# Kernel tuning notes

Hardware: AMD Instinct MI355X
Metric: run time of the kernel (lower is better)

Reference implementation:

```python
import jax, jax.numpy as jnp
import numpy as np

N = 50000
E = 800000
H = 128

def setup_inputs() -> dict:
    key = jax.random.key(0)
    ks = jax.random.split(key, 12)
    s = 1.0 / np.sqrt(H)
    inp = {
        "x": jax.random.normal(ks[0], (N, H), dtype=jnp.float32),
        "edge_index": jax.random.randint(ks[1], (2, E), 0, N, dtype=jnp.int64),
        "edge_attr": jax.random.normal(ks[2], (E, H), dtype=jnp.float32),
        # linear_edge: Linear(3H, H)
        "We": jax.random.uniform(ks[3], (3 * H, H), jnp.float32, -s, s),
        "be": jnp.zeros((H,), jnp.float32),
        # attention_layer.W: Linear(H, H)
        "Wg": jax.random.uniform(ks[4], (H, H), jnp.float32, -s, s),
        "bg": jnp.zeros((H,), jnp.float32),
        # attention_layer.a: Linear(2H, 1)
        "Wa": jax.random.uniform(ks[5], (2 * H, 1), jnp.float32, -s, s),
        "ba": jnp.zeros((1,), jnp.float32),
        # linear_out: Linear(H, H)
        "Wo": jax.random.uniform(ks[6], (H, H), jnp.float32, -s, s),
        "bo": jnp.zeros((H,), jnp.float32),
    }
    return inp


def reference(x, edge_index, edge_attr, We, be, Wg, bg, Wa, ba, Wo, bo):
    # PyG MessagePassing (flow=source_to_target): j = edge_index[0] (source),
    # i = edge_index[1] (target); aggregation scatters to edge_index[1].
    src = edge_index[0]
    dst = edge_index[1]

    # message: SiLU(Linear(cat[x_i, x_j, edge_attr]))  -- split We to avoid a [E,3H] concat
    m = jax.nn.silu(x[dst] @ We[:H] + x[src] @ We[H:2 * H] + edge_attr @ We[2 * H:] + be)  # [E,H]
    agg = jax.ops.segment_sum(m, dst, num_segments=N)  # [N,H] scatter-add aggregate

    # GraphAttentionLayer: row, col = edge_index -> row=edge_index[0], col=edge_index[1]
    h = agg @ Wg + bg  # [N,H]
    score = jax.nn.leaky_relu(h[src] @ Wa[:H] + h[dst] @ Wa[H:] + ba, negative_slope=0.2)  # [E,1]
    # softmax over the last dim of size 1 -> all ones (faithful to original); dropout off (eval)
    alpha = jax.nn.softmax(score, axis=-1)  # [E,1]
    attn_out = jax.ops.segment_sum(alpha * h[dst], src, num_segments=N)  # [N,H]

    return attn_out @ Wo + bo  # linear_out
```

## Files before the change

### kernel.cpp

```cpp
#include <hip/hip_runtime.h>

#define N_NODES 50000
#define N_EDGES 800000

typedef unsigned short u16;
typedef unsigned int u32;
typedef __attribute__((ext_vector_type(8))) short short8;
typedef __attribute__((ext_vector_type(4))) float f32x4;
typedef __attribute__((ext_vector_type(2))) float f32x2;

__device__ __forceinline__ u16 f2bf(float f) {
    union { float f; u32 u; } v; v.f = f;
    u32 r = v.u + 0x7FFFu + ((v.u >> 16) & 1u);
    return (u16)(r >> 16);
}

__device__ __forceinline__ float bf2f(u16 h) {
    union { u32 u; float f; } v; v.u = ((u32)h) << 16;
    return v.f;
}

__global__ __launch_bounds__(256) void compute_wc(const float* __restrict__ Wg,
                                                  const float* __restrict__ bg,
                                                  const float* __restrict__ Wo,
                                                  float* __restrict__ Wc,
                                                  float* __restrict__ bc) {
    int b = blockIdx.x;
    if (b < 8) {
        for (int i = 0; i < 8; ++i) {
            int o = b * 2048 + i * 256 + threadIdx.x;
            int k = o >> 7, n = o & 127;
            float s = 0.f;
            for (int j = 0; j < 128; ++j) s += Wg[k * 128 + j] * Wo[j * 128 + n];
            Wc[o] = s;
        }
    } else if (threadIdx.x < 128) {
        int n = threadIdx.x;
        float s = 0.f;
        for (int j = 0; j < 128; ++j) s += bg[j] * Wo[j * 128 + n];
        bc[n] = s;
    }
}

__global__ __launch_bounds__(256) void pack_all(const float* __restrict__ We,
                                                const float* __restrict__ Wc,
                                                u16* __restrict__ PB1,
                                                u16* __restrict__ PBe,
                                                u16* __restrict__ PBc) {
    int bid = blockIdx.x;
    int job = bid >> 3;
    int t = bid & 7;
    const float* src; u16* dst; int slotBase, CH;
    if (job == 0)      { src = We;         dst = PB1; slotBase = 0; CH = 4; }
    else if (job == 1) { src = We + 32768; dst = PBe; slotBase = 0; CH = 8; }
    else if (job == 2) { src = We + 16384; dst = PBe; slotBase = 4; CH = 8; }
    else               { src = Wc;         dst = PBc; slotBase = 0; CH = 4; }
    int c = threadIdx.x >> 6;
    int lane = threadIdx.x & 63;
    int q = lane >> 4, n = lane & 15;
    const float* s = src + (size_t)(c * 32 + q * 8) * 128 + t * 16 + n;
    u16* dp = dst + (((size_t)(t * CH + slotBase + c) * 64 + lane) * 8);
#pragma unroll
    for (int j = 0; j < 8; ++j) dp[j] = f2bf(s[(size_t)j * 128]);
}

__global__ __launch_bounds__(256) void cast_bf16(const float* __restrict__ x,
                                                 u16* __restrict__ X2) {
    size_t i = (size_t)(blockIdx.x * 256 + threadIdx.x) * 8;
    f32x4 v0 = *(const f32x4*)(x + i);
    f32x4 v1 = *(const f32x4*)(x + i + 4);
    short8 o;
#pragma unroll
    for (int j = 0; j < 4; ++j) { o[j] = (short)f2bf(v0[j]); o[4 + j] = (short)f2bf(v1[j]); }
    *(short8*)(X2 + i) = o;
}

__global__ __launch_bounds__(256) void hist_kernel(const int* __restrict__ srcIdx,
                                                   const int* __restrict__ dstIdx,
                                                   int* __restrict__ degD,
                                                   int* __restrict__ degS) {
    int e = blockIdx.x * 256 + threadIdx.x;
    if (e >= N_EDGES) return;
    atomicAdd(&degD[dstIdx[e]], 1);
    atomicAdd(&degS[srcIdx[e]], 1);
}

__global__ __launch_bounds__(256) void scan_kernel(const int* __restrict__ degD,
                                                   const int* __restrict__ degS,
                                                   int* __restrict__ offD, int* __restrict__ curD,
                                                   int* __restrict__ offS, int* __restrict__ curS) {
    const int* deg = blockIdx.x ? degS : degD;
    int* off = blockIdx.x ? offS : offD;
    int* cur = blockIdx.x ? curS : curD;
    __shared__ int buf[256];
    const int CHUNK = 196;
    int tid = threadIdx.x;
    int s0 = tid * CHUNK, s1 = s0 + CHUNK;
    if (s1 > N_NODES) s1 = N_NODES;
    int s = 0;
    for (int i = s0; i < s1; ++i) s += deg[i];
    buf[tid] = s;
    __syncthreads();
    for (int o = 1; o < 256; o <<= 1) {
        int v = (tid >= o) ? buf[tid - o] : 0;
        __syncthreads();
        buf[tid] += v;
        __syncthreads();
    }
    int run = (tid > 0) ? buf[tid - 1] : 0;
    for (int i = s0; i < s1; ++i) {
        off[i] = run;
        cur[i] = run;
        run += deg[i];
    }
    if (tid == 255) off[N_NODES] = buf[255];
}

__global__ __launch_bounds__(256) void scatter_kernel(const int* __restrict__ srcIdx,
                                                      const int* __restrict__ dstIdx,
                                                      int* __restrict__ curD,
                                                      int* __restrict__ curS,
                                                      int2* __restrict__ sdP,
                                                      int* __restrict__ ss_dst) {
    int e = blockIdx.x * 256 + threadIdx.x;
    if (e >= N_EDGES) return;
    int s = srcIdx[e], d = dstIdx[e];
    int p = atomicAdd(&curD[d], 1);
    sdP[p] = make_int2(e, s);
    int p2 = atomicAdd(&curS[s], 1);
    ss_dst[p2] = d;
}

__global__ __launch_bounds__(256) void gemm_mfma(const void* __restrict__ Ap,
                                                 const u16* __restrict__ PB,
                                                 const float* __restrict__ bias,
                                                 const float* __restrict__ bias2,
                                                 const int* __restrict__ rowdeg,
                                                 void* __restrict__ outp,
                                                 int M, int Ctiles, int flags) {
    int tid = threadIdx.x;
    int wave = tid >> 6;
    int lane = tid & 63;
    int strip = blockIdx.x * 4 + wave;
    int row0 = strip * 16;
    if (row0 >= M) return;
    int q = lane >> 4, n = lane & 15;
    int C = Ctiles * 16;

    short8 a[4];
    if (flags & 2) {
        const u16* ap = (const u16*)Ap + (size_t)(row0 + n) * 128 + q * 8;
#pragma unroll
        for (int c = 0; c < 4; ++c) a[c] = *(const short8*)(ap + c * 32);
    } else {
        const float* ap = (const float*)Ap + (size_t)(row0 + n) * 128 + q * 8;
#pragma unroll
        for (int c = 0; c < 4; ++c) {
            f32x4 f0 = *(const f32x4*)(ap + c * 32);
            f32x4 f1 = *(const f32x4*)(ap + c * 32 + 4);
            short8 t;
#pragma unroll
            for (int j = 0; j < 4; ++j) {
                t[j] = (short)f2bf(f0[j]);
                t[4 + j] = (short)f2bf(f1[j]);
            }
            a[c] = t;
        }
    }

    float rb[4] = {0.f, 0.f, 0.f, 0.f};
    if (flags & 4) {
#pragma unroll
        for (int r = 0; r < 4; ++r) rb[r] = (float)rowdeg[row0 + q * 4 + r];
    }

    for (int t = 0; t < Ctiles; ++t) {
        f32x4 acc = {0.f, 0.f, 0.f, 0.f};
#pragma unroll
        for (int c = 0; c < 4; ++c) {
            short8 b = *(const short8*)(PB + (((size_t)t * 4 + c) * 64 + lane) * 8);
            acc = __builtin_amdgcn_mfma_f32_16x16x32_bf16(a[c], b, acc, 0, 0, 0);
        }
        int col = t * 16 + n;
        float bv = bias ? bias[col] : 0.f;
        float b2 = (flags & 4) ? bias2[col] : 0.f;
#pragma unroll
        for (int r = 0; r < 4; ++r) {
            int row = row0 + q * 4 + r;
            float v = acc[r] + bv + rb[r] * b2;
            if (flags & 1)
                ((u16*)outp)[(size_t)row * C + col] = f2bf(v);
            else
                ((float*)outp)[(size_t)row * C + col] = v;
        }
    }
}

__global__ __launch_bounds__(256) void agg_fused(const float* __restrict__ EA,
                                                 const u16* __restrict__ X2,
                                                 const u16* __restrict__ PBe,
                                                 const int* __restrict__ offD,
                                                 const int2* __restrict__ sdP,
                                                 const u16* __restrict__ T1a,
                                                 u16* __restrict__ agg) {
    int tid = threadIdx.x;
    int wave = tid >> 6;
    int lane = tid & 63;
    int node = blockIdx.x * 2 + (wave >> 1);
    if (node >= N_NODES) return;
    int cg = wave & 1;
    int q = lane >> 4, n = lane & 15;
    int segS = offD[node], segE = offD[node + 1];
    const u16* pb = PBe + (size_t)cg * 16384;

    float g1[4], rowAcc[4];
#pragma unroll
    for (int t = 0; t < 4; ++t) {
        g1[t] = bf2f(T1a[(size_t)node * 128 + (cg * 4 + t) * 16 + n]);
        rowAcc[t] = 0.f;
    }

    for (int base = segS; base < segE; base += 16) {
        int er = base + n;
        if (er > segE - 1) er = segE - 1;
        int2 es = sdP[er];
        const float* ap = EA + (size_t)es.x * 128 + q * 8;
        const u16* xp = X2 + (size_t)es.y * 128 + q * 8;
        short8 a[8];
#pragma unroll
        for (int c = 0; c < 4; ++c) {
            f32x4 f0 = *(const f32x4*)(ap + c * 32);
            f32x4 f1 = *(const f32x4*)(ap + c * 32 + 4);
            short8 t;
#pragma unroll
            for (int j = 0; j < 4; ++j) {
                t[j] = (short)f2bf(f0[j]);
                t[4 + j] = (short)f2bf(f1[j]);
            }
            a[c] = t;
            a[4 + c] = *(const short8*)(xp + c * 32);
        }
        bool val[4];
#pragma unroll
        for (int r = 0; r < 4; ++r) val[r] = (base + q * 4 + r) < segE;

#pragma unroll
        for (int t = 0; t < 4; ++t) {
            f32x4 acc = {0.f, 0.f, 0.f, 0.f};
#pragma unroll
            for (int c = 0; c < 8; ++c) {
                short8 b = *(const short8*)(pb + (((size_t)t * 8 + c) * 64 + lane) * 8);
                acc = __builtin_amdgcn_mfma_f32_16x16x32_bf16(a[c], b, acc, 0, 0, 0);
            }
#pragma unroll
            for (int r = 0; r < 4; ++r) {
                float v = acc[r] + g1[t];
                float m = v * __builtin_amdgcn_rcpf(1.f + __expf(-v));
                rowAcc[t] += val[r] ? m : 0.f;
            }
        }
    }
#pragma unroll
    for (int t = 0; t < 4; ++t) {
        float v = rowAcc[t];
        v += __shfl_xor(v, 16, 64);
        v += __shfl_xor(v, 32, 64);
        if (lane < 16) agg[(size_t)node * 128 + (cg * 4 + t) * 16 + lane] = f2bf(v);
    }
}

__global__ __launch_bounds__(256) void attn_gather(const int* __restrict__ offS,
                                                   const int* __restrict__ ss_dst,
                                                   const u16* __restrict__ hsrc,
                                                   float* __restrict__ attn) {
    int tid = threadIdx.x;
    int wave = tid >> 6;
    int lane = tid & 63;
    int node = blockIdx.x * 4 + wave;
    if (node >= N_NODES) return;
    int e0 = offS[node], e1 = offS[node + 1];
    float a0 = 0.f, a1 = 0.f;
    for (int base = e0; base < e1; base += 64) {
        int m = e1 - base;
        if (m > 64) m = 64;
        int ii = lane < m ? lane : m - 1;
        int myIdx = ss_dst[base + ii];
        int j = 0;
        for (; j + 4 <= m; j += 4) {
            int d0 = __shfl(myIdx, j, 64);
            int d1 = __shfl(myIdx, j + 1, 64);
            int d2 = __shfl(myIdx, j + 2, 64);
            int d3 = __shfl(myIdx, j + 3, 64);
            u32 h0 = *(const u32*)(hsrc + (size_t)d0 * 128 + lane * 2);
            u32 h1 = *(const u32*)(hsrc + (size_t)d1 * 128 + lane * 2);
            u32 h2 = *(const u32*)(hsrc + (size_t)d2 * 128 + lane * 2);
            u32 h3 = *(const u32*)(hsrc + (size_t)d3 * 128 + lane * 2);
            a0 += bf2f((u16)(h0 & 0xFFFFu)) + bf2f((u16)(h1 & 0xFFFFu)) +
                  bf2f((u16)(h2 & 0xFFFFu)) + bf2f((u16)(h3 & 0xFFFFu));
            a1 += bf2f((u16)(h0 >> 16)) + bf2f((u16)(h1 >> 16)) +
                  bf2f((u16)(h2 >> 16)) + bf2f((u16)(h3 >> 16));
        }
        for (; j < m; ++j) {
            int d = __shfl(myIdx, j, 64);
            u32 h = *(const u32*)(hsrc + (size_t)d * 128 + lane * 2);
            a0 += bf2f((u16)(h & 0xFFFFu));
            a1 += bf2f((u16)(h >> 16));
        }
    }
    f32x2 o;
    o[0] = a0;
    o[1] = a1;
    *(f32x2*)(attn + (size_t)node * 128 + lane * 2) = o;
}

extern "C" void kernel_launch(void* const* d_in, const int* in_sizes, int n_in,
                              void* d_out, int out_size, void* d_ws, size_t ws_size,
                              hipStream_t stream) {
    const float* x  = (const float*)d_in[0];
    const int* ei   = (const int*)d_in[1];
    const float* ea = (const float*)d_in[2];
    const float* We = (const float*)d_in[3];
    const float* be = (const float*)d_in[4];
    const float* Wg = (const float*)d_in[5];
    const float* bg = (const float*)d_in[6];
    const float* Wo = (const float*)d_in[9];
    const float* bo = (const float*)d_in[10];
    float* out = (float*)d_out;

    const int* srcIdx = ei;
    const int* dstIdx = ei + N_EDGES;

    char* ws = (char*)d_ws;
    u16*   PB1    = (u16*)(ws + 0);
    u16*   PBe    = (u16*)(ws + 32768);
    u16*   PBc    = (u16*)(ws + 98304);
    float* Wc     = (float*)(ws + 131072);
    float* bc     = (float*)(ws + 196608);
    u16*   T1a    = (u16*)(ws + 262144);
    u16*   X2     = (u16*)(ws + 13062144);
    float* attn   = (float*)(ws + 262144);
    u16*   agg    = (u16*)(ws + 25862144);
    int*   degD   = (int*)(ws + 38662144);
    int*   degS   = (int*)(ws + 38862144);
    int*   offD   = (int*)(ws + 39062144);
    int*   offS   = (int*)(ws + 39262160);
    int*   curD   = (int*)(ws + 39462176);
    int*   curS   = (int*)(ws + 39662176);
    int2*  sdP    = (int2*)(ws + 39862176);
    int*   ss_dst = (int*)(ws + 46262176);

    hipMemsetAsync(degD, 0, 400000, stream);

    compute_wc<<<9, 256, 0, stream>>>(Wg, bg, Wo, Wc, bc);
    pack_all<<<32, 256, 0, stream>>>(We, Wc, PB1, PBe, PBc);

    hist_kernel<<<3125, 256, 0, stream>>>(srcIdx, dstIdx, degD, degS);
    scan_kernel<<<2, 256, 0, stream>>>(degD, degS, offD, curD, offS, curS);
    scatter_kernel<<<3125, 256, 0, stream>>>(srcIdx, dstIdx, curD, curS, sdP, ss_dst);

    cast_bf16<<<3125, 256, 0, stream>>>(x, X2);

    gemm_mfma<<<782, 256, 0, stream>>>(x, PB1, be, nullptr, nullptr, T1a, N_NODES, 8, 1);

    agg_fused<<<25000, 256, 0, stream>>>(ea, X2, PBe, offD, sdP, T1a, agg);

    attn_gather<<<12500, 256, 0, stream>>>(offS, ss_dst, agg, attn);

    gemm_mfma<<<782, 256, 0, stream>>>(attn, PBc, bo, bc, degS, out, N_NODES, 8, 4);

    (void)in_sizes; (void)n_in; (void)out_size; (void)ws_size;
}
```

Baseline: 1.253 ms.

## Switch edge aggregation to fixed 16-edge tiles with segmented atomic scatter

Edge messages are now computed per fixed 16-edge tile over the dst-sorted edge list, with x_dst included as a third K-block in the MFMA. Previously each node was processed separately using a precomputed node GEMM T1a. Partial sums of consecutive edges that share a destination are combined in registers and then scattered into an fp32 agg buffer with atomics. This removes per-node load imbalance and the padding of short segments, but adds float atomics and extra gather traffic. Preprocessing (x cast, weight packing, zeroing, Wc compute) is merged into one prep kernel, and attn_gather now reads fp32 agg in 16-edge chunks.

After: 1.230 ms. About the same (-1.8%).

```diff
diff --git a/kernel.cpp b/kernel.cpp
--- a/kernel.cpp
+++ b/kernel.cpp
@@ -2,6 +2,7 @@
 
 #define N_NODES 50000
 #define N_EDGES 800000
+#define N_TILES 50000
 
 typedef unsigned short u16;
 typedef unsigned int u32;
@@ -20,59 +21,64 @@
     return v.f;
 }
 
-__global__ __launch_bounds__(256) void compute_wc(const float* __restrict__ Wg,
-                                                  const float* __restrict__ bg,
-                                                  const float* __restrict__ Wo,
-                                                  float* __restrict__ Wc,
-                                                  float* __restrict__ bc) {
-    int b = blockIdx.x;
-    if (b < 8) {
+__global__ __launch_bounds__(256) void prep_kernel(const float* __restrict__ x,
+                                                   const float* __restrict__ We,
+                                                   const float* __restrict__ Wg,
+                                                   const float* __restrict__ bg,
+                                                   const float* __restrict__ Wo,
+                                                   u16* __restrict__ Xbf,
+                                                   u16* __restrict__ PBe,
+                                                   u16* __restrict__ PBc,
+                                                   float* __restrict__ bc,
+                                                   float* __restrict__ aggF,
+                                                   int* __restrict__ degZ) {
+    int b = blockIdx.x, tid = threadIdx.x;
+    if (b < 3125) {
+        size_t i = ((size_t)b * 256 + tid) * 8;
+        f32x4 v0 = *(const f32x4*)(x + i);
+        f32x4 v1 = *(const f32x4*)(x + i + 4);
+        short8 o;
+#pragma unroll
+        for (int j = 0; j < 4; ++j) { o[j] = (short)f2bf(v0[j]); o[4 + j] = (short)f2bf(v1[j]); }
+        *(short8*)(Xbf + i) = o;
+    } else if (b < 4725) {
+        int bb = b - 3125;
+#pragma unroll
+        for (int k = 0; k < 4; ++k) {
+            int idx4 = bb * 1024 + k * 256 + tid;
+            if (idx4 < 1600000) ((f32x4*)aggF)[idx4] = (f32x4){0.f, 0.f, 0.f, 0.f};
+        }
+    } else if (b < 4823) {
+        int idx4 = (b - 4725) * 256 + tid;
+        if (idx4 < 25000) ((int4*)degZ)[idx4] = make_int4(0, 0, 0, 0);
+    } else if (b < 4847) {
+        int bb = b - 4823;
+        int jb = bb >> 3, t = bb & 7;
+        const float* src = (jb == 0) ? We + 32768 : (jb == 1) ? We + 16384 : We;
+        int c = tid >> 6, lane = tid & 63, q = lane >> 4, n = lane & 15;
+        int slot = jb * 4 + c;
+        const float* s = src + (size_t)(c * 32 + q * 8) * 128 + t * 16 + n;
+        u16* dp = PBe + (((size_t)(t * 12 + slot) * 64 + lane) * 8);
+#pragma unroll
+        for (int j = 0; j < 8; ++j) dp[j] = f2bf(s[(size_t)j * 128]);
+    } else if (b < 4855) {
+        int w = b - 4847;
         for (int i = 0; i < 8; ++i) {
-            int o = b * 2048 + i * 256 + threadIdx.x;
+            int o = w * 2048 + i * 256 + tid;
             int k = o >> 7, n = o & 127;
             float s = 0.f;
             for (int j = 0; j < 128; ++j) s += Wg[k * 128 + j] * Wo[j * 128 + n];
-            Wc[o] = s;
-        }
-    } else if (threadIdx.x < 128) {
-        int n = threadIdx.x;
-        float s = 0.f;
-        for (int j = 0; j < 128; ++j) s += bg[j] * Wo[j * 128 + n];
-        bc[n] = s;
-    }
-}
-
-__global__ __launch_bounds__(256) void pack_all(const float* __restrict__ We,
-                                                const float* __restrict__ Wc,
-                                                u16* __restrict__ PB1,
-                                                u16* __restrict__ PBe,
-                                                u16* __restrict__ PBc) {
-    int bid = blockIdx.x;
-    int job = bid >> 3;
-    int t = bid & 7;
-    const float* src; u16* dst; int slotBase, CH;
-    if (job == 0)      { src = We;         dst = PB1; slotBase = 0; CH = 4; }
-    else if (job == 1) { src = We + 32768; dst = PBe; slotBase = 0; CH = 8; }
-    else if (job == 2) { src = We + 16384; dst = PBe; slotBase = 4; CH = 8; }
-    else               { src = Wc;         dst = PBc; slotBase = 0; CH = 4; }
-    int c = threadIdx.x >> 6;
-    int lane = threadIdx.x & 63;
-    int q = lane >> 4, n = lane & 15;
-    const float* s = src + (size_t)(c * 32 + q * 8) * 128 + t * 16 + n;
-    u16* dp = dst + (((size_t)(t * CH + slotBase + c) * 64 + lane) * 8);
-#pragma unroll
-    for (int j = 0; j < 8; ++j) dp[j] = f2bf(s[(size_t)j * 128]);
-}
-
-__global__ __launch_bounds__(256) void cast_bf16(const float* __restrict__ x,
-                                                 u16* __restrict__ X2) {
-    size_t i = (size_t)(blockIdx.x * 256 + threadIdx.x) * 8;
-    f32x4 v0 = *(const f32x4*)(x + i);
-    f32x4 v1 = *(const f32x4*)(x + i + 4);
-    short8 o;
-#pragma unroll
-    for (int j = 0; j < 4; ++j) { o[j] = (short)f2bf(v0[j]); o[4 + j] = (short)f2bf(v1[j]); }
-    *(short8*)(X2 + i) = o;
+            int t = n >> 4, c = k >> 5, q = (k >> 3) & 3, j8 = k & 7;
+            int ln = (q << 4) | (n & 15);
+            PBc[(((size_t)(t * 4 + c) * 64 + ln) * 8) + j8] = f2bf(s);
+        }
+    } else {
+        if (tid < 128) {
+            float s = 0.f;
+            for (int j = 0; j < 128; ++j) s += bg[j] * Wo[j * 128 + tid];
+            bc[tid] = s;
+        }
+    }
 }
 
 __global__ __launch_bounds__(256) void hist_kernel(const int* __restrict__ srcIdx,
@@ -120,24 +126,24 @@
                                                       const int* __restrict__ dstIdx,
                                                       int* __restrict__ curD,
                                                       int* __restrict__ curS,
-                                                      int2* __restrict__ sdP,
+                                                      int4* __restrict__ sdP,
                                                       int* __restrict__ ss_dst) {
     int e = blockIdx.x * 256 + threadIdx.x;
     if (e >= N_EDGES) return;
     int s = srcIdx[e], d = dstIdx[e];
     int p = atomicAdd(&curD[d], 1);
-    sdP[p] = make_int2(e, s);
+    sdP[p] = make_int4(e, s, d, 0);
     int p2 = atomicAdd(&curS[s], 1);
     ss_dst[p2] = d;
 }
 
-__global__ __launch_bounds__(256) void gemm_mfma(const void* __restrict__ Ap,
+__global__ __launch_bounds__(256) void gemm_mfma(const float* __restrict__ Ap,
                                                  const u16* __restrict__ PB,
                                                  const float* __restrict__ bias,
                                                  const float* __restrict__ bias2,
                                                  const int* __restrict__ rowdeg,
-                                                 void* __restrict__ outp,
-                                                 int M, int Ctiles, int flags) {
+                                                 float* __restrict__ outp,
+                                                 int M, int Ctiles) {
     int tid = threadIdx.x;
     int wave = tid >> 6;
     int lane = tid & 63;
@@ -148,31 +154,23 @@
     int C = Ctiles * 16;
 
     short8 a[4];
-    if (flags & 2) {
-        const u16* ap = (const u16*)Ap + (size_t)(row0 + n) * 128 + q * 8;
-#pragma unroll
-        for (int c = 0; c < 4; ++c) a[c] = *(const short8*)(ap + c * 32);
-    } else {
-        const float* ap = (const float*)Ap + (size_t)(row0 + n) * 128 + q * 8;
-#pragma unroll
-        for (int c = 0; c < 4; ++c) {
-            f32x4 f0 = *(const f32x4*)(ap + c * 32);
-            f32x4 f1 = *(const f32x4*)(ap + c * 32 + 4);
-            short8 t;
-#pragma unroll
-            for (int j = 0; j < 4; ++j) {
-                t[j] = (short)f2bf(f0[j]);
-                t[4 + j] = (short)f2bf(f1[j]);
-            }
-            a[c] = t;
-        }
-    }
-
-    float rb[4] = {0.f, 0.f, 0.f, 0.f};
-    if (flags & 4) {
-#pragma unroll
-        for (int r = 0; r < 4; ++r) rb[r] = (float)rowdeg[row0 + q * 4 + r];
-    }
+    const float* ap = Ap + (size_t)(row0 + n) * 128 + q * 8;
+#pragma unroll
+    for (int c = 0; c < 4; ++c) {
+        f32x4 f0 = *(const f32x4*)(ap + c * 32);
+        f32x4 f1 = *(const f32x4*)(ap + c * 32 + 4);
+        short8 t;
+#pragma unroll
+        for (int j = 0; j < 4; ++j) {
+            t[j] = (short)f2bf(f0[j]);
+            t[4 + j] = (short)f2bf(f1[j]);
+        }
+        a[c] = t;
+    }
+
+    float rb[4];
+#pragma unroll
+    for (int r = 0; r < 4; ++r) rb[r] = (float)rowdeg[row0 + q * 4 + r];
 
     for (int t = 0; t < Ctiles; ++t) {
         f32x4 acc = {0.f, 0.f, 0.f, 0.f};
@@ -182,97 +180,88 @@
             acc = __builtin_amdgcn_mfma_f32_16x16x32_bf16(a[c], b, acc, 0, 0, 0);
         }
         int col = t * 16 + n;
-        float bv = bias ? bias[col] : 0.f;
-        float b2 = (flags & 4) ? bias2[col] : 0.f;
+        float bv = bias[col];
+        float b2 = bias2[col];
 #pragma unroll
         for (int r = 0; r < 4; ++r) {
             int row = row0 + q * 4 + r;
-            float v = acc[r] + bv + rb[r] * b2;
-            if (flags & 1)
-                ((u16*)outp)[(size_t)row * C + col] = f2bf(v);
-            else
-                ((float*)outp)[(size_t)row * C + col] = v;
+            outp[(size_t)row * C + col] = acc[r] + bv + rb[r] * b2;
         }
     }
 }
 
 __global__ __launch_bounds__(256) void agg_fused(const float* __restrict__ EA,
-                                                 const u16* __restrict__ X2,
+                                                 const u16* __restrict__ Xbf,
                                                  const u16* __restrict__ PBe,
-                                                 const int* __restrict__ offD,
-                                                 const int2* __restrict__ sdP,
-                                                 const u16* __restrict__ T1a,
-                                                 u16* __restrict__ agg) {
+                                                 const float* __restrict__ be,
+                                                 const int4* __restrict__ sdP,
+                                                 float* __restrict__ aggF) {
     int tid = threadIdx.x;
     int wave = tid >> 6;
     int lane = tid & 63;
-    int node = blockIdx.x * 2 + (wave >> 1);
-    if (node >= N_NODES) return;
-    int cg = wave & 1;
+    int tile = blockIdx.x * 4 + wave;
     int q = lane >> 4, n = lane & 15;
-    int segS = offD[node], segE = offD[node + 1];
-    const u16* pb = PBe + (size_t)cg * 16384;
-
-    float g1[4], rowAcc[4];
-#pragma unroll
-    for (int t = 0; t < 4; ++t) {
-        g1[t] = bf2f(T1a[(size_t)node * 128 + (cg * 4 + t) * 16 + n]);
-        rowAcc[t] = 0.f;
-    }
-
-    for (int base = segS; base < segE; base += 16) {
-        int er = base + n;
-        if (er > segE - 1) er = segE - 1;
-        int2 es = sdP[er];
-        const float* ap = EA + (size_t)es.x * 128 + q * 8;
-        const u16* xp = X2 + (size_t)es.y * 128 + q * 8;
-        short8 a[8];
-#pragma unroll
-        for (int c = 0; c < 4; ++c) {
-            f32x4 f0 = *(const f32x4*)(ap + c * 32);
-            f32x4 f1 = *(const f32x4*)(ap + c * 32 + 4);
-            short8 t;
-#pragma unroll
-            for (int j = 0; j < 4; ++j) {
-                t[j] = (short)f2bf(f0[j]);
-                t[4 + j] = (short)f2bf(f1[j]);
-            }
-            a[c] = t;
-            a[4 + c] = *(const short8*)(xp + c * 32);
-        }
-        bool val[4];
-#pragma unroll
-        for (int r = 0; r < 4; ++r) val[r] = (base + q * 4 + r) < segE;
-
-#pragma unroll
-        for (int t = 0; t < 4; ++t) {
-            f32x4 acc = {0.f, 0.f, 0.f, 0.f};
-#pragma unroll
-            for (int c = 0; c < 8; ++c) {
-                short8 b = *(const short8*)(pb + (((size_t)t * 8 + c) * 64 + lane) * 8);
-                acc = __builtin_amdgcn_mfma_f32_16x16x32_bf16(a[c], b, acc, 0, 0, 0);
-            }
-#pragma unroll
-            for (int r = 0; r < 4; ++r) {
-                float v = acc[r] + g1[t];
-                float m = v * __builtin_amdgcn_rcpf(1.f + __expf(-v));
-                rowAcc[t] += val[r] ? m : 0.f;
-            }
-        }
-    }
-#pragma unroll
-    for (int t = 0; t < 4; ++t) {
-        float v = rowAcc[t];
-        v += __shfl_xor(v, 16, 64);
-        v += __shfl_xor(v, 32, 64);
-        if (lane < 16) agg[(size_t)node * 128 + (cg * 4 + t) * 16 + lane] = f2bf(v);
+
+    int4 es = sdP[tile * 16 + n];
+    const float* ap = EA + (size_t)es.x * 128 + q * 8;
+    const u16* xs = Xbf + (size_t)es.y * 128 + q * 8;
+    const u16* xd = Xbf + (size_t)es.z * 128 + q * 8;
+
+    short8 a[12];
+#pragma unroll
+    for (int c = 0; c < 4; ++c) {
+        f32x4 f0 = *(const f32x4*)(ap + c * 32);
+        f32x4 f1 = *(const f32x4*)(ap + c * 32 + 4);
+        short8 t;
+#pragma unroll
+        for (int j = 0; j < 4; ++j) {
+            t[j] = (short)f2bf(f0[j]);
+            t[4 + j] = (short)f2bf(f1[j]);
+        }
+        a[c] = t;
+        a[4 + c] = *(const short8*)(xs + c * 32);
+        a[8 + c] = *(const short8*)(xd + c * 32);
+    }
+
+    int d0 = __shfl(es.z, q * 4 + 0, 64);
+    int d1 = __shfl(es.z, q * 4 + 1, 64);
+    int d2 = __shfl(es.z, q * 4 + 2, 64);
+    int d3 = __shfl(es.z, q * 4 + 3, 64);
+    bool c1 = (d1 == d0), c2 = (d2 == d1), c3 = (d3 == d2);
+
+    float bb[8];
+#pragma unroll
+    for (int t = 0; t < 8; ++t) bb[t] = be[t * 16 + n];
+
+#pragma unroll
+    for (int t = 0; t < 8; ++t) {
+        f32x4 acc = {0.f, 0.f, 0.f, 0.f};
+#pragma unroll
+        for (int c = 0; c < 12; ++c) {
+            short8 b = *(const short8*)(PBe + (((size_t)t * 12 + c) * 64 + lane) * 8);
+            acc = __builtin_amdgcn_mfma_f32_16x16x32_bf16(a[c], b, acc, 0, 0, 0);
+        }
+        float v0 = acc[0] + bb[t], v1 = acc[1] + bb[t], v2 = acc[2] + bb[t], v3 = acc[3] + bb[t];
+        v0 *= __builtin_amdgcn_rcpf(1.f + __expf(-v0));
+        v1 *= __builtin_amdgcn_rcpf(1.f + __expf(-v1));
+        v2 *= __builtin_amdgcn_rcpf(1.f + __expf(-v2));
+        v3 *= __builtin_amdgcn_rcpf(1.f + __expf(-v3));
+        float s0 = v0;
+        float s1 = v1 + (c1 ? s0 : 0.f);
+        float s2 = v2 + (c2 ? s1 : 0.f);
+        float s3 = v3 + (c3 ? s2 : 0.f);
+        float* basep = aggF + t * 16 + n;
+        if (!c1) atomicAdd(basep + (size_t)d0 * 128, s0);
+        if (!c2) atomicAdd(basep + (size_t)d1 * 128, s1);
+        if (!c3) atomicAdd(basep + (size_t)d2 * 128, s2);
+        atomicAdd(basep + (size_t)d3 * 128, s3);
     }
 }
 
 __global__ __launch_bounds__(256) void attn_gather(const int* __restrict__ offS,
                                                    const int* __restrict__ ss_dst,
-                                                   const u16* __restrict__ hsrc,
-                                                   float* __restrict__ attn) {
+                                                   const float* __restrict__ aggF,
+                                                   float* __restrict__ attnB) {
     int tid = threadIdx.x;
     int wave = tid >> 6;
     int lane = tid & 63;
@@ -280,37 +269,25 @@
     if (node >= N_NODES) return;
     int e0 = offS[node], e1 = offS[node + 1];
     float a0 = 0.f, a1 = 0.f;
-    for (int base = e0; base < e1; base += 64) {
+    for (int base = e0; base < e1; base += 16) {
         int m = e1 - base;
-        if (m > 64) m = 64;
-        int ii = lane < m ? lane : m - 1;
-        int myIdx = ss_dst[base + ii];
-        int j = 0;
-        for (; j + 4 <= m; j += 4) {
-            int d0 = __shfl(myIdx, j, 64);
-            int d1 = __shfl(myIdx, j + 1, 64);
-            int d2 = __shfl(myIdx, j + 2, 64);
-            int d3 = __shfl(myIdx, j + 3, 64);
-            u32 h0 = *(const u32*)(hsrc + (size_t)d0 * 128 + lane * 2);
-            u32 h1 = *(const u32*)(hsrc + (size_t)d1 * 128 + lane * 2);
-            u32 h2 = *(const u32*)(hsrc + (size_t)d2 * 128 + lane * 2);
-            u32 h3 = *(const u32*)(hsrc + (size_t)d3 * 128 + lane * 2);
-            a0 += bf2f((u16)(h0 & 0xFFFFu)) + bf2f((u16)(h1 & 0xFFFFu)) +
-                  bf2f((u16)(h2 & 0xFFFFu)) + bf2f((u16)(h3 & 0xFFFFu));
-            a1 += bf2f((u16)(h0 >> 16)) + bf2f((u16)(h1 >> 16)) +
-                  bf2f((u16)(h2 >> 16)) + bf2f((u16)(h3 >> 16));
-        }
-        for (; j < m; ++j) {
-            int d = __shfl(myIdx, j, 64);
-            u32 h = *(const u32*)(hsrc + (size_t)d * 128 + lane * 2);
-            a0 += bf2f((u16)(h & 0xFFFFu));
-            a1 += bf2f((u16)(h >> 16));
+        if (m > 16) m = 16;
+        int ii = base + (lane & 15);
+        if (ii > e1 - 1) ii = e1 - 1;
+        int idxv = ss_dst[ii];
+#pragma unroll
+        for (int i = 0; i < 16; ++i) {
+            bool val = i < m;
+            int d = __shfl(idxv, val ? i : 0, 64);
+            f32x2 h = *(const f32x2*)(aggF + (size_t)d * 128 + lane * 2);
+            a0 += val ? h[0] : 0.f;
+            a1 += val ? h[1] : 0.f;
         }
     }
     f32x2 o;
     o[0] = a0;
     o[1] = a1;
-    *(f32x2*)(attn + (size_t)node * 128 + lane * 2) = o;
+    *(f32x2*)(attnB + (size_t)node * 128 + lane * 2) = o;
 }
 
 extern "C" void kernel_launch(void* const* d_in, const int* in_sizes, int n_in,
@@ -331,42 +308,32 @@
     const int* dstIdx = ei + N_EDGES;
 
     char* ws = (char*)d_ws;
-    u16*   PB1    = (u16*)(ws + 0);
-    u16*   PBe    = (u16*)(ws + 32768);
+    u16*   PBe    = (u16*)(ws + 0);
     u16*   PBc    = (u16*)(ws + 98304);
-    float* Wc     = (float*)(ws + 131072);
-    float* bc     = (float*)(ws + 196608);
-    u16*   T1a    = (u16*)(ws + 262144);
-    u16*   X2     = (u16*)(ws + 13062144);
-    float* attn   = (float*)(ws + 262144);
-    u16*   agg    = (u16*)(ws + 25862144);
-    int*   degD   = (int*)(ws + 38662144);
-    int*   degS   = (int*)(ws + 38862144);
-    int*   offD   = (int*)(ws + 39062144);
-    int*   offS   = (int*)(ws + 39262160);
-    int*   curD   = (int*)(ws + 39462176);
-    int*   curS   = (int*)(ws + 39662176);
-    int2*  sdP    = (int2*)(ws + 39862176);
-    int*   ss_dst = (int*)(ws + 46262176);
-
-    hipMemsetAsync(degD, 0, 400000, stream);
-
-    compute_wc<<<9, 256, 0, stream>>>(Wg, bg, Wo, Wc, bc);
-    pack_all<<<32, 256, 0, stream>>>(We, Wc, PB1, PBe, PBc);
+    float* bc     = (float*)(ws + 131072);
+    u16*   Xbf    = (u16*)(ws + 262144);
+    int4*  sdP    = (int4*)(ws + 13062144);
+    float* attnB  = (float*)(ws + 262144);
+    int*   ss_dst = (int*)(ws + 25862144);
+    float* aggF   = (float*)(ws + 29062144);
+    int*   degD   = (int*)(ws + 54662144);
+    int*   degS   = (int*)(ws + 54862144);
+    int*   offD   = (int*)(ws + 55062144);
+    int*   offS   = (int*)(ws + 55262160);
+    int*   curD   = (int*)(ws + 55462176);
+    int*   curS   = (int*)(ws + 55662176);
+
+    prep_kernel<<<4856, 256, 0, stream>>>(x, We, Wg, bg, Wo, Xbf, PBe, PBc, bc, aggF, degD);
 
     hist_kernel<<<3125, 256, 0, stream>>>(srcIdx, dstIdx, degD, degS);
     scan_kernel<<<2, 256, 0, stream>>>(degD, degS, offD, curD, offS, curS);
     scatter_kernel<<<3125, 256, 0, stream>>>(srcIdx, dstIdx, curD, curS, sdP, ss_dst);
 
-    cast_bf16<<<3125, 256, 0, stream>>>(x, X2);
-
-    gemm_mfma<<<782, 256, 0, stream>>>(x, PB1, be, nullptr, nullptr, T1a, N_NODES, 8, 1);
-
-    agg_fused<<<25000, 256, 0, stream>>>(ea, X2, PBe, offD, sdP, T1a, agg);
-
-    attn_gather<<<12500, 256, 0, stream>>>(offS, ss_dst, agg, attn);
-
-    gemm_mfma<<<782, 256, 0, stream>>>(attn, PBc, bo, bc, degS, out, N_NODES, 8, 4);
+    agg_fused<<<12500, 256, 0, stream>>>(ea, Xbf, PBe, be, sdP, aggF);
+
+    attn_gather<<<12500, 256, 0, stream>>>(offS, ss_dst, aggF, attnB);
+
+    gemm_mfma<<<782, 256, 0, stream>>>(attnB, PBc, bo, bc, degS, out, N_NODES, 8);
 
     (void)in_sizes; (void)n_in; (void)out_size; (void)ws_size;
 }
```
